# Kernel tuning notes

Hardware: AMD Instinct MI355X
Metric: run time of the kernel (lower is better)

## Reference

```python
import jax, jax.numpy as jnp
import numpy as np

B, S, H, P, L, O, E = 32, 1024, 256, 96, 200, 200, 64
N_EULER = 4


def setup_inputs() -> dict:
    key = jax.random.key(0)
    ks = jax.random.split(key, 20)
    def w(k, shape, fan_in):
        return jax.random.normal(k, shape, dtype=jnp.float32) / np.float32(np.sqrt(fan_in))
    return {
        'eco_data': jax.random.normal(ks[0], (B, E), dtype=jnp.float32),
        'tran_data': jax.random.normal(ks[1], (B, S, H), dtype=jnp.float32),
        'tran_data_label': jax.random.normal(ks[2], (B, P, 1), dtype=jnp.float32),
        'time_x': jax.random.uniform(ks[3], (B, S, 1), dtype=jnp.float32),
        'time_y': jax.random.uniform(ks[4], (B, P, 1), dtype=jnp.float32),
        'alpha': jnp.ones((1,), dtype=jnp.float32),
        'W_eco': w(ks[5], (E, H), E), 'b_eco': jnp.zeros((H,), jnp.float32),
        'W_in': w(ks[6], (3, H, L), H), 'W_t': w(ks[7], (3, 1, L), 1), 'b_in': jnp.zeros((3, L), jnp.float32),
        'W_f1': w(ks[8], (3, L, O), L), 'b_f1': jnp.zeros((3, O), jnp.float32),
        'W_f2': w(ks[9], (3, O, L), O), 'b_f2': jnp.zeros((3, L), jnp.float32),
        'W_out': w(ks[10], (3, L, H), L), 'b_out': jnp.zeros((3, H), jnp.float32),
        'W_lin': w(ks[11], (H, P), H), 'b_lin': jnp.zeros((P,), jnp.float32),
    }


def reference(eco_data, tran_data, tran_data_label, time_x, time_y, alpha,
              W_eco, b_eco, W_in, W_t, b_in, W_f1, b_f1, W_f2, b_f2,
              W_out, b_out, W_lin, b_lin):
    S_ = tran_data.shape[1]
    # eco_model: linear encoder [B, E] -> [B, H]
    eco_vec = eco_data @ W_eco + b_eco
    # time features over the observed window (concat then slice, per original)
    time_f = jnp.concatenate([time_x, time_y], axis=1)[:, :S_, :]  # [B, S, 1]
    # ODE_RNN for Q/K/V, stacked on k=3: encode -> Euler ODE solve -> readout
    h = jnp.tanh(jnp.einsum('bsh,khl->kbsl', tran_data, W_in)
                 + jnp.einsum('bst,ktl->kbsl', time_f, W_t)
                 + b_in[:, None, None, :])  # [3, B, S, L]
    dt = jnp.float32(1.0 / N_EULER)
    for _ in range(N_EULER):  # fixed-step Euler solve of tanh-MLP vector field
        hid = jnp.tanh(jnp.einsum('kbsl,klo->kbso', h, W_f1) + b_f1[:, None, None, :])
        f = jnp.einsum('kbso,kol->kbsl', hid, W_f2) + b_f2[:, None, None, :]
        h = h + dt * f
    qkv = (jnp.einsum('kbsl,klh->kbsh', h, W_out) + b_out[:, None, None, :]
           + eco_vec[None, :, None, :])  # [3, B, S, H]
    # zero out padded timesteps (last channel == 0 means padding)
    mask = jnp.where(tran_data[:, :, -1] == 0, 0.0, 1.0)[None, :, :, None]
    qkv = qkv * mask
    Q, K, V = qkv[0], qkv[1], qkv[2]
    scale = jnp.float32(1.0 / np.sqrt(H))
    scores = jnp.einsum('bqh,bkh->bqk', Q, K) * scale  # [B, S, S]
    attn = jax.nn.softmax(scores, axis=-1)
    ctx = jnp.einsum('bqk,bkh->bqh', attn, V)  # [B, S, H]
    out = ctx @ W_lin + b_lin  # [B, S, P]
    return out
```

## Files before the change

kernel.cpp:

```cpp
#include <hip/hip_runtime.h>

constexpr int Bc = 32, Sc = 1024, Hc = 256, Pc = 96, Lc = 200, Oc = 200, Ec = 64;
constexpr int Mtot = Bc * Sc;
constexpr float DT = 0.25f;
constexpr int KP = 224;

enum { MODE_ENC = 0, MODE_QKV = 3, MODE_OUT = 4, MODE_BF16OUT = 5 };

typedef short bf16x8 __attribute__((ext_vector_type(8)));
typedef float f32x4 __attribute__((ext_vector_type(4)));
typedef unsigned short u16x8 __attribute__((ext_vector_type(8)));
typedef unsigned int u32x2 __attribute__((ext_vector_type(2)));

__device__ inline unsigned short f2bf(float x) {
    union { float f; unsigned int u; } v; v.f = x;
    unsigned int r = v.u + 0x7FFFu + ((v.u >> 16) & 1u);
    return (unsigned short)(r >> 16);
}
__device__ inline float bf2f(unsigned short x) {
    union { unsigned int u; float f; } v; v.u = ((unsigned int)x) << 16;
    return v.f;
}
__device__ inline float fast_tanh(float x) {
    float e = __expf(2.f * x);
    float r = __frcp_rn(e + 1.f);
    return fmaf(-2.f, r, 1.f);
}
__device__ inline unsigned int cvt_pk_bf16(float a, float b) {
    unsigned int r;
    asm("v_cvt_pk_bf16_f32 %0, %1, %2" : "=v"(r) : "v"(a), "v"(b));
    return r;
}

__global__ __launch_bounds__(256) void eco_kernel(
    const float* __restrict__ eco_data, const float* __restrict__ W_eco,
    const float* __restrict__ b_eco, float* __restrict__ eco_vec)
{
    const int b = blockIdx.x, h = threadIdx.x;
    float acc = b_eco[h];
    #pragma unroll
    for (int e = 0; e < Ec; e++)
        acc = fmaf(eco_data[b * Ec + e], W_eco[(size_t)e * Hc + h], acc);
    eco_vec[(size_t)b * Hc + h] = acc;
}

__global__ void wtrans_all(
    const float* __restrict__ W_in, const float* __restrict__ W_f1,
    const float* __restrict__ W_f2, const float* __restrict__ W_out,
    const float* __restrict__ W_lin,
    unsigned short* __restrict__ WinT, unsigned short* __restrict__ Wf1T,
    unsigned short* __restrict__ Wf2T, unsigned short* __restrict__ WoutT,
    unsigned short* __restrict__ WlinT)
{
    const int z = blockIdx.z;
    const int n = blockIdx.x * 16 + threadIdx.x;
    const int k = blockIdx.y * 16 + threadIdx.y;

    const float* W; unsigned short* WT;
    int K, N, Kpad, Npad;
    if (z < 3)       { W = W_in  + (size_t)z * 256 * 200;       WT = WinT  + (size_t)z * 256 * 256;       K = 256; N = 200; Kpad = 256; Npad = 256; }
    else if (z < 6)  { W = W_f1  + (size_t)(z - 3) * 200 * 200; WT = Wf1T  + (size_t)(z - 3) * 224 * 256; K = 200; N = 200; Kpad = 224; Npad = 256; }
    else if (z < 9)  { W = W_f2  + (size_t)(z - 6) * 200 * 200; WT = Wf2T  + (size_t)(z - 6) * 224 * 256; K = 200; N = 200; Kpad = 224; Npad = 256; }
    else if (z < 12) { W = W_out + (size_t)(z - 9) * 200 * 256; WT = WoutT + (size_t)(z - 9) * 224 * 256; K = 200; N = 256; Kpad = 224; Npad = 256; }
    else             { W = W_lin;                               WT = WlinT;                               K = 256; N =  96; Kpad = 256; Npad = 128; }

    if (n >= Npad || k >= Kpad) return;
    float v = (n < N && k < K) ? W[(size_t)k * N + n] : 0.f;
    WT[(size_t)n * Kpad + k] = f2bf(v);
}

template <int MODE, typename TA>
__global__ __launch_bounds__(256) void mfma_gemm(
    const TA* __restrict__ A, const unsigned short* __restrict__ WT,
    const float* __restrict__ bias, void* __restrict__ Cv,
    int M, int N, int K, int Kpad,
    size_t aStrideZ, size_t wStrideZ, size_t bStrideZ, size_t cStrideZ,
    const float* __restrict__ timev, const float* __restrict__ wtv,
    const float* __restrict__ eco, const float* __restrict__ trandat,
    unsigned short* __restrict__ Ck, unsigned short* __restrict__ Cvt)
{
    constexpr int LDS_S = 40;
    constexpr int HALF = 128 * LDS_S;
    __shared__ unsigned short SM[4 * HALF];

    const int tid = threadIdx.x;
    const int z = blockIdx.z;
    const int m0 = blockIdx.y * 128;
    const int n0 = blockIdx.x * 128;

    A    += (size_t)z * aStrideZ;
    WT   += (size_t)z * wStrideZ;
    bias += (size_t)z * bStrideZ;
    float* Cf = (float*)Cv + (size_t)z * cStrideZ;
    unsigned short* Cu = (unsigned short*)Cv + (size_t)z * cStrideZ;
    const float* wtp = wtv ? (wtv + (size_t)z * Lc) : nullptr;

    const int lane = tid & 63, wave = tid >> 6;
    const int wm = (wave & 1) * 64, wn = (wave >> 1) * 64;
    const int fm = lane & 15, fq = lane >> 4;

    f32x4 acc[4][4];
    #pragma unroll
    for (int i = 0; i < 4; i++)
        #pragma unroll
        for (int j = 0; j < 4; j++)
            acc[i][j] = (f32x4){0.f, 0.f, 0.f, 0.f};

    float4  paf[4];
    ushort4 pau[4];
    u16x8   pb[2];

    auto LOAD = [&](int k0) {
        #pragma unroll
        for (int i = 0; i < 4; i++) {
            const int f = i * 256 + tid;
            const int row = f >> 3, kq = f & 7;
            if constexpr (sizeof(TA) == 4)
                paf[i] = *(const float4*)((const float*)A + (size_t)(m0 + row) * K + k0 + kq * 4);
            else
                pau[i] = *(const ushort4*)((const unsigned short*)A + (size_t)(m0 + row) * K + k0 + kq * 4);
        }
        #pragma unroll
        for (int i = 0; i < 2; i++) {
            const int f = i * 256 + tid;
            const int row = f >> 2, q = f & 3;
            pb[i] = *(const u16x8*)(WT + (size_t)(n0 + row) * Kpad + k0 + q * 8);
        }
    };
    auto STORE = [&](int buf) {
        unsigned short* Asd = SM + buf * 2 * HALF;
        unsigned short* Bsd = Asd + HALF;
        #pragma unroll
        for (int i = 0; i < 4; i++) {
            const int f = i * 256 + tid;
            const int row = f >> 3, kq = f & 7;
            ushort4 s;
            if constexpr (sizeof(TA) == 4) {
                s.x = f2bf(paf[i].x); s.y = f2bf(paf[i].y);
                s.z = f2bf(paf[i].z); s.w = f2bf(paf[i].w);
            } else {
                s = pau[i];
            }
            *(ushort4*)&Asd[row * LDS_S + kq * 4] = s;
        }
        #pragma unroll
        for (int i = 0; i < 2; i++) {
            const int f = i * 256 + tid;
            const int row = f >> 2, q = f & 3;
            *(u16x8*)&Bsd[row * LDS_S + q * 8] = pb[i];
        }
    };

    const int nk = K >> 5;
    LOAD(0);
    STORE(0);

    for (int ki = 0; ki < nk; ki++) {
        __syncthreads();
        const unsigned short* Asr = SM + (ki & 1) * 2 * HALF;
        const unsigned short* Bsr = Asr + HALF;

        if (ki + 1 < nk) LOAD((ki + 1) * 32);

        bf16x8 af[4], bfr[4];
        #pragma unroll
        for (int mi = 0; mi < 4; mi++)
            af[mi] = *(const bf16x8*)&Asr[(wm + mi * 16 + fm) * LDS_S + fq * 8];
        #pragma unroll
        for (int nj = 0; nj < 4; nj++)
            bfr[nj] = *(const bf16x8*)&Bsr[(wn + nj * 16 + fm) * LDS_S + fq * 8];
        #pragma unroll
        for (int mi = 0; mi < 4; mi++)
            #pragma unroll
            for (int nj = 0; nj < 4; nj++)
                acc[mi][nj] = __builtin_amdgcn_mfma_f32_16x16x32_bf16(
                    af[mi], bfr[nj], acc[mi][nj], 0, 0, 0);

        if (ki + 1 < nk) STORE((ki + 1) & 1);
    }

    if (MODE == MODE_QKV && z == 2) {
        constexpr int BSTR = 136;
        const int bq = m0 >> 10, sq0 = m0 & (Sc - 1);
        const int myhalf = wn >> 6;
        #pragma unroll
        for (int half = 0; half < 2; half++) {
            __syncthreads();
            if (myhalf == half) {
                #pragma unroll
                for (int mi = 0; mi < 4; mi++)
                    #pragma unroll
                    for (int nj = 0; nj < 4; nj++) {
                        const int nn = n0 + wn + nj * 16 + fm;
                        const float bv = bias[nn];
                        const float ev = eco[(size_t)bq * Hc + nn];
                        #pragma unroll
                        for (int r = 0; r < 4; r++) {
                            const int mm = m0 + wm + mi * 16 + fq * 4 + r;
                            float v = acc[mi][nj][r] + bv + ev;
                            if (trandat[(size_t)mm * Hc + (Hc - 1)] == 0.f) v = 0.f;
                            SM[(nj * 16 + fm) * BSTR + wm + mi * 16 + fq * 4 + r] = f2bf(v);
                        }
                    }
            }
            __syncthreads();
            #pragma unroll
            for (int i = 0; i < 4; i++) {
                const int vv = i * 256 + tid;
                const int nl = vv >> 4, vc = vv & 15;
                *(u16x8*)&Cvt[((size_t)bq * Hc + n0 + half * 64 + nl) * Sc + sq0 + vc * 8] =
                    *(const u16x8*)&SM[nl * BSTR + vc * 8];
            }
        }
        return;
    }

    #pragma unroll
    for (int mi = 0; mi < 4; mi++) {
        #pragma unroll
        for (int nj = 0; nj < 4; nj++) {
            const int nn = n0 + wn + nj * 16 + fm;
            if (nn >= N) continue;
            const float bv = (MODE == MODE_BF16OUT) ? 0.f
                           : ((MODE == MODE_ENC && nn >= Lc) ? 0.f : bias[nn]);
            #pragma unroll
            for (int r = 0; r < 4; r++) {
                const int mm = m0 + wm + mi * 16 + fq * 4 + r;
                float v = acc[mi][nj][r] + bv;
                if (MODE == MODE_ENC) {
                    float vv = (nn < Lc) ? fast_tanh(v + timev[mm] * wtp[nn]) : 0.f;
                    Cu[(size_t)mm * N + nn] = f2bf(vv);
                } else if (MODE == MODE_QKV) {
                    v += eco[(size_t)(mm >> 10) * Hc + nn];
                    if (trandat[(size_t)mm * Hc + (Hc - 1)] == 0.f) v = 0.f;
                    if (z == 0)      ((unsigned short*)Cv)[(size_t)mm * Hc + nn] = f2bf(v * 0.0625f);
                    else             Ck[(size_t)mm * Hc + nn] = f2bf(v);
                } else if (MODE == MODE_BF16OUT) {
                    Cu[(size_t)mm * N + nn] = f2bf(v);
                } else {
                    Cf[(size_t)mm * N + nn] = v;
                }
            }
        }
    }
}

__global__ __launch_bounds__(512, 2) void euler_fused(
    unsigned short* __restrict__ hg,
    const unsigned short* __restrict__ W1,
    const unsigned short* __restrict__ W2,
    const float* __restrict__ b1g, const float* __restrict__ b2g)
{
    constexpr int HS = 232;
    constexpr int WS = 40;
    extern __shared__ unsigned short lds[];
    unsigned short* hs  = lds;
    unsigned short* wsb[2] = { lds + 29696, lds + 38656 };
    unsigned short* hcb[2] = { lds + 47616, lds + 52736 };
    float* bs = (float*)(lds + 57856);

    const int tid = threadIdx.x;
    const int z = blockIdx.y;
    const int m0 = blockIdx.x * 128;
    unsigned short* hrow = hg + ((size_t)z * Mtot + m0) * KP;
    const unsigned short* W1z = W1 + (size_t)z * 256 * KP;
    const unsigned short* W2z = W2 + (size_t)z * 256 * KP;

    const int lane = tid & 63, w = tid >> 6;
    const int wm = (w & 3) * 32, wn = (w >> 2) * 112;
    const int fm = lane & 15, fq = lane >> 4;

    const int sr = tid >> 2, sq = tid & 3;
    const bool s2 = (tid < 384);

    if (tid < 448) {
        float v;
        if (tid < 224) v = (tid < Oc) ? b1g[z * Oc + tid] : 0.f;
        else { const int t = tid - 224; v = (t < Lc) ? b2g[z * Lc + t] : 0.f; }
        bs[tid] = v;
    }

    u16x8 pr0, pr1;
    pr0 = *(const u16x8*)&W1z[sr * KP + sq * 8];
    if (s2) pr1 = *(const u16x8*)&W1z[(sr + 128) * KP + sq * 8];

    #pragma unroll
    for (int i = 0; i < 7; i++) {
        const int f = i * 512 + tid;
        const int r = f / 28, c = (f % 28) * 8;
        *(u16x8*)&hs[r * HS + c] = *(const u16x8*)&hrow[(size_t)r * KP + c];
    }

    for (int it = 0; it < 4; it++) {
        __syncthreads();
        *(u16x8*)&wsb[0][sr * WS + sq * 8] = pr0;
        if (s2) *(u16x8*)&wsb[0][(sr + 128) * WS + sq * 8] = pr1;
        pr0 = *(const u16x8*)&W1z[sr * KP + 32 + sq * 8];
        if (s2) pr1 = *(const u16x8*)&W1z[(sr + 128) * KP + 32 + sq * 8];
        __syncthreads();

        f32x4 acc[2][7];
        #pragma unroll
        for (int mi = 0; mi < 2; mi++)
            #pragma unroll
            for (int nj = 0; nj < 7; nj++)
                acc[mi][nj] = (f32x4){0.f, 0.f, 0.f, 0.f};

        for (int k = 0; k < 7; k++) {
            if (k < 6) {
                unsigned short* wb = wsb[(k + 1) & 1];
                *(u16x8*)&wb[sr * WS + sq * 8] = pr0;
                if (s2) *(u16x8*)&wb[(sr + 128) * WS + sq * 8] = pr1;
                const unsigned short* src = (k + 2 < 7) ? (W1z + (k + 2) * 32) : W2z;
                pr0 = *(const u16x8*)&src[sr * KP + sq * 8];
                if (s2) pr1 = *(const u16x8*)&src[(sr + 128) * KP + sq * 8];
            }
            const unsigned short* wr = wsb[k & 1];
            bf16x8 af[2], bfr[7];
            #pragma unroll
            for (int mi = 0; mi < 2; mi++)
                af[mi] = *(const bf16x8*)&hs[(wm + mi * 16 + fm) * HS + k * 32 + fq * 8];
            #pragma unroll
            for (int nj = 0; nj < 7; nj++)
                bfr[nj] = *(const bf16x8*)&wr[(wn + nj * 16 + fm) * WS + fq * 8];
            #pragma unroll
            for (int mi = 0; mi < 2; mi++)
                #pragma unroll
                for (int nj = 0; nj < 7; nj++)
                    acc[mi][nj] = __builtin_amdgcn_mfma_f32_16x16x32_bf16(
                        bfr[nj], af[mi], acc[mi][nj], 0, 0, 0);
            __syncthreads();
        }

        unsigned int hidp[2][7][2];
        #pragma unroll
        for (int nj = 0; nj < 7; nj++) {
            const f32x4 b1v = *(const f32x4*)&bs[wn + nj * 16 + fq * 4];
            #pragma unroll
            for (int mi = 0; mi < 2; mi++) {
                const float t0 = fast_tanh(acc[mi][nj][0] + b1v[0]);
                const float t1 = fast_tanh(acc[mi][nj][1] + b1v[1]);
                const float t2 = fast_tanh(acc[mi][nj][2] + b1v[2]);
                const float t3 = fast_tanh(acc[mi][nj][3] + b1v[3]);
                hidp[mi][nj][0] = cvt_pk_bf16(t0, t1);
                hidp[mi][nj][1] = cvt_pk_bf16(t2, t3);
            }
        }

        {
            *(u16x8*)&wsb[0][sr * WS + sq * 8] = pr0;
            if (s2) *(u16x8*)&wsb[0][(sr + 128) * WS + sq * 8] = pr1;
            pr0 = *(const u16x8*)&W2z[sr * KP + 32 + sq * 8];
            if (s2) pr1 = *(const u16x8*)&W2z[(sr + 128) * KP + 32 + sq * 8];
            #pragma unroll
            for (int t2 = 0; t2 < 2; t2++) {
                const int c0 = t2 * 16;
                if (c0 >= wn && c0 < wn + 112) {
                    const int nj = (c0 - wn) >> 4;
                    #pragma unroll
                    for (int mi = 0; mi < 2; mi++) {
                        u32x2 p; p[0] = hidp[mi][nj][0]; p[1] = hidp[mi][nj][1];
                        *(u32x2*)&hcb[0][(wm + mi * 16 + fm) * WS + t2 * 16 + fq * 4] = p;
                    }
                }
            }
        }
        __syncthreads();

        f32x4 fac[2][7];
        #pragma unroll
        for (int mi = 0; mi < 2; mi++)
            #pragma unroll
            for (int nj = 0; nj < 7; nj++)
                fac[mi][nj] = (f32x4){0.f, 0.f, 0.f, 0.f};

        for (int k = 0; k < 7; k++) {
            if (k < 6) {
                unsigned short* wb = wsb[(k + 1) & 1];
                unsigned short* hb = hcb[(k + 1) & 1];
                *(u16x8*)&wb[sr * WS + sq * 8] = pr0;
                if (s2) *(u16x8*)&wb[(sr + 128) * WS + sq * 8] = pr1;
                if (k + 2 < 7) {
                    pr0 = *(const u16x8*)&W2z[sr * KP + (k + 2) * 32 + sq * 8];
                    if (s2) pr1 = *(const u16x8*)&W2z[(sr + 128) * KP + (k + 2) * 32 + sq * 8];
                } else if (it != 3) {
                    pr0 = *(const u16x8*)&W1z[sr * KP + sq * 8];
                    if (s2) pr1 = *(const u16x8*)&W1z[(sr + 128) * KP + sq * 8];
                }
                #pragma unroll
                for (int t2 = 0; t2 < 2; t2++) {
                    const int c0 = (k + 1) * 32 + t2 * 16;
                    if (c0 >= wn && c0 < wn + 112) {
                        const int nj = (c0 - wn) >> 4;
                        #pragma unroll
                        for (int mi = 0; mi < 2; mi++) {
                            u32x2 p; p[0] = hidp[mi][nj][0]; p[1] = hidp[mi][nj][1];
                            *(u32x2*)&hb[(wm + mi * 16 + fm) * WS + t2 * 16 + fq * 4] = p;
                        }
                    }
                }
            }
            const unsigned short* wr = wsb[k & 1];
            const unsigned short* hr = hcb[k & 1];
            bf16x8 af2[2], bf2[7];
            #pragma unroll
            for (int mi = 0; mi < 2; mi++)
                af2[mi] = *(const bf16x8*)&hr[(wm + mi * 16 + fm) * WS + fq * 8];
            #pragma unroll
            for (int nj = 0; nj < 7; nj++)
                bf2[nj] = *(const bf16x8*)&wr[(wn + nj * 16 + fm) * WS + fq * 8];
            #pragma unroll
            for (int mi = 0; mi < 2; mi++)
                #pragma unroll
                for (int nj = 0; nj < 7; nj++)
                    fac[mi][nj] = __builtin_amdgcn_mfma_f32_16x16x32_bf16(
                        bf2[nj], af2[mi], fac[mi][nj], 0, 0, 0);
            __syncthreads();
        }

        #pragma unroll
        for (int nj = 0; nj < 7; nj++) {
            const int n = wn + nj * 16 + fq * 4;
            const f32x4 b2v = *(const f32x4*)&bs[224 + n];
            #pragma unroll
            for (int mi = 0; mi < 2; mi++) {
                const int m = wm + mi * 16 + fm;
                const ushort4 hv = *(const ushort4*)&hs[m * HS + n];
                const float v0 = bf2f(hv.x) + DT * (fac[mi][nj][0] + b2v[0]);
                const float v1 = bf2f(hv.y) + DT * (fac[mi][nj][1] + b2v[1]);
                const float v2 = bf2f(hv.z) + DT * (fac[mi][nj][2] + b2v[2]);
                const float v3 = bf2f(hv.w) + DT * (fac[mi][nj][3] + b2v[3]);
                u32x2 p; p[0] = cvt_pk_bf16(v0, v1); p[1] = cvt_pk_bf16(v2, v3);
                *(u32x2*)&hs[m * HS + n] = p;
            }
        }
    }

    __syncthreads();
    #pragma unroll
    for (int i = 0; i < 7; i++) {
        const int f = i * 512 + tid;
        const int r = f / 28, c = (f % 28) * 8;
        *(u16x8*)&hrow[(size_t)r * KP + c] = *(const u16x8*)&hs[r * HS + c];
    }
}

__global__ __launch_bounds__(512) void flash_attn(
    const unsigned short* __restrict__ Qb, const unsigned short* __restrict__ Kb,
    const unsigned short* __restrict__ VT, unsigned short* __restrict__ ctx)
{
    constexpr int QS = 264;
    constexpr int KS = 264;
    constexpr int VS = 72;
    constexpr int PS = 72;
    extern __shared__ unsigned short lds[];
    unsigned short* qs = lds;
    unsigned short* ks = lds + 128 * QS;
    unsigned short* vs = lds + 128 * QS + 64 * KS;
    unsigned short* ps = lds + 128 * QS + 64 * KS + 256 * VS;

    const int tid = threadIdx.x;
    const int b = blockIdx.y, q0 = blockIdx.x * 128;
    const int lane = tid & 63, w = tid >> 6;
    const int fm = lane & 15, fq = lane >> 4;
    unsigned short* psw = ps + w * 16 * PS;

    const unsigned short* Qp = Qb + (size_t)b * Sc * Hc;
    const unsigned short* Kp = Kb + (size_t)b * Sc * Hc;
    const unsigned short* Vp = VT + (size_t)b * Hc * Sc;

    #pragma unroll
    for (int i = 0; i < 8; i++) {
        const int v = i * 512 + tid;
        *(u16x8*)&qs[(v >> 5) * QS + (v & 31) * 8] =
            *(const u16x8*)&Qp[(size_t)(q0 + (v >> 5)) * Hc + (v & 31) * 8];
    }

    f32x4 of[16];
    #pragma unroll
    for (int nj = 0; nj < 16; nj++) of[nj] = (f32x4){0.f, 0.f, 0.f, 0.f};
    float lrun[4] = {0.f, 0.f, 0.f, 0.f};

    for (int c = 0; c < 16; c++) {
        __syncthreads();
        const int s0 = c * 64;
        #pragma unroll
        for (int i = 0; i < 4; i++) {
            const int v = i * 512 + tid;
            *(u16x8*)&ks[(v >> 5) * KS + (v & 31) * 8] =
                *(const u16x8*)&Kp[(size_t)(s0 + (v >> 5)) * Hc + (v & 31) * 8];
            *(u16x8*)&vs[(v >> 3) * VS + (v & 7) * 8] =
                *(const u16x8*)&Vp[(size_t)(v >> 3) * Sc + s0 + (v & 7) * 8];
        }
        __syncthreads();

        f32x4 sc[4];
        #pragma unroll
        for (int nj = 0; nj < 4; nj++) sc[nj] = (f32x4){0.f, 0.f, 0.f, 0.f};
        #pragma unroll
        for (int kc = 0; kc < 8; kc++) {
            const bf16x8 aq = *(const bf16x8*)&qs[(w * 16 + fm) * QS + kc * 32 + fq * 8];
            #pragma unroll
            for (int nj = 0; nj < 4; nj++) {
                const bf16x8 bk = *(const bf16x8*)&ks[(nj * 16 + fm) * KS + kc * 32 + fq * 8];
                sc[nj] = __builtin_amdgcn_mfma_f32_16x16x32_bf16(aq, bk, sc[nj], 0, 0, 0);
            }
        }

        float rsum[4] = {0.f, 0.f, 0.f, 0.f};
        #pragma unroll
        for (int nj = 0; nj < 4; nj++)
            #pragma unroll
            for (int r = 0; r < 4; r++) {
                const float p = __expf(sc[nj][r]);
                rsum[r] += p;
                psw[(fq * 4 + r) * PS + nj * 16 + fm] = f2bf(p);
            }
        #pragma unroll
        for (int r = 0; r < 4; r++) {
            float s = rsum[r];
            #pragma unroll
            for (int o = 8; o > 0; o >>= 1) s += __shfl_xor(s, o, 64);
            lrun[r] += s;
        }

        #pragma unroll
        for (int t = 0; t < 2; t++) {
            const bf16x8 ap = *(const bf16x8*)&psw[fm * PS + t * 32 + fq * 8];
            #pragma unroll
            for (int nj = 0; nj < 16; nj++) {
                const bf16x8 bv = *(const bf16x8*)&vs[(nj * 16 + fm) * VS + t * 32 + fq * 8];
                of[nj] = __builtin_amdgcn_mfma_f32_16x16x32_bf16(ap, bv, of[nj], 0, 0, 0);
            }
        }
    }

    float inv[4];
    #pragma unroll
    for (int r = 0; r < 4; r++) inv[r] = __frcp_rn(lrun[r]);
    #pragma unroll
    for (int nj = 0; nj < 16; nj++)
        #pragma unroll
        for (int r = 0; r < 4; r++)
            ctx[((size_t)b * Sc + q0 + w * 16 + fq * 4 + r) * Hc + nj * 16 + fm] =
                f2bf(of[nj][r] * inv[r]);
}

extern "C" void kernel_launch(void* const* d_in, const int* in_sizes, int n_in,
                              void* d_out, int out_size, void* d_ws, size_t ws_size,
                              hipStream_t stream)
{
    const float* eco_data = (const float*)d_in[0];
    const float* tran     = (const float*)d_in[1];
    const float* time_x   = (const float*)d_in[3];
    const float* W_eco    = (const float*)d_in[6];
    const float* b_eco    = (const float*)d_in[7];
    const float* W_in     = (const float*)d_in[8];
    const float* W_t      = (const float*)d_in[9];
    const float* b_in     = (const float*)d_in[10];
    const float* W_f1     = (const float*)d_in[11];
    const float* b_f1     = (const float*)d_in[12];
    const float* W_f2     = (const float*)d_in[13];
    const float* b_f2     = (const float*)d_in[14];
    const float* W_out    = (const float*)d_in[15];
    const float* b_out    = (const float*)d_in[16];
    const float* W_lin    = (const float*)d_in[17];
    const float* b_lin    = (const float*)d_in[18];
    float* out = (float*)d_out;

    float* eco_vec = (float*)d_ws;
    unsigned short* hpad = (unsigned short*)(eco_vec + 8192);
    unsigned short* Qb = hpad + (size_t)3 * Mtot * KP;
    unsigned short* Kb = Qb + (size_t)Mtot * Hc;
    unsigned short* VT = Kb + (size_t)Mtot * Hc;
    unsigned short* P  = VT + (size_t)Mtot * Hc;
    unsigned short* WinT  = P + (size_t)Mtot * Sc;
    unsigned short* Wf1T  = WinT  + (size_t)3 * 256 * 256;
    unsigned short* Wf2T  = Wf1T  + (size_t)3 * 256 * KP;
    unsigned short* WoutT = Wf2T  + (size_t)3 * 256 * KP;
    unsigned short* WlinT = WoutT + (size_t)3 * 256 * KP;
    unsigned short* ctxb = hpad;

    constexpr int EULER_LDS = 57856 * 2 + 448 * 4;
    static_assert(EULER_LDS == 117504, "euler lds");
    hipFuncSetAttribute((const void*)euler_fused,
                        hipFuncAttributeMaxDynamicSharedMemorySize, EULER_LDS);
    constexpr int FLASH_LDS = (128 * 264 + 64 * 264 + 256 * 72 + 8 * 16 * 72) * 2;
    static_assert(FLASH_LDS == 156672, "flash lds");
    hipFuncSetAttribute((const void*)flash_attn,
                        hipFuncAttributeMaxDynamicSharedMemorySize, FLASH_LDS);

    eco_kernel<<<Bc, Hc, 0, stream>>>(eco_data, W_eco, b_eco, eco_vec);

    wtrans_all<<<dim3(16, 16, 13), dim3(16, 16), 0, stream>>>(
        W_in, W_f1, W_f2, W_out, W_lin, WinT, Wf1T, Wf2T, WoutT, WlinT);

    const dim3 blk(256);

    mfma_gemm<MODE_ENC, float><<<dim3(2, 256, 3), blk, 0, stream>>>(
        tran, WinT, b_in, hpad, Mtot, KP, Hc, 256,
        0, 65536, Lc, (size_t)Mtot * KP, time_x, W_t, nullptr, nullptr, nullptr, nullptr);

    euler_fused<<<dim3(Mtot / 128, 3), 512, EULER_LDS, stream>>>(
        hpad, Wf1T, Wf2T, b_f1, b_f2);

    mfma_gemm<MODE_QKV, unsigned short><<<dim3(2, 256, 3), blk, 0, stream>>>(
        hpad, WoutT, b_out, Qb, Mtot, Hc, KP, KP,
        (size_t)Mtot * KP, 57344, Hc, 0, nullptr, nullptr, eco_vec, tran, Kb, VT);

    flash_attn<<<dim3(8, 32), 512, FLASH_LDS, stream>>>(Qb, Kb, VT, ctxb);

    mfma_gemm<MODE_OUT, unsigned short><<<dim3(1, 256, 1), blk, 0, stream>>>(
        ctxb, WlinT, b_lin, out, Mtot, Pc, Hc, 256,
        0, 0, 0, 0, nullptr, nullptr, nullptr, nullptr, nullptr, nullptr);
}
```

Before: 458.8 us.

## Double-buffer K/V tiles via registers and keep Q fragments in registers in flash attention

```diff
diff --git a/kernel.cpp b/kernel.cpp
--- a/kernel.cpp
+++ b/kernel.cpp
@@ -449,15 +449,12 @@
     const unsigned short* __restrict__ Qb, const unsigned short* __restrict__ Kb,
     const unsigned short* __restrict__ VT, unsigned short* __restrict__ ctx)
 {
-    constexpr int QS = 264;
     constexpr int KS = 264;
     constexpr int VS = 72;
     constexpr int PS = 72;
+    constexpr int BUF = 64 * KS + 256 * VS;
     extern __shared__ unsigned short lds[];
-    unsigned short* qs = lds;
-    unsigned short* ks = lds + 128 * QS;
-    unsigned short* vs = lds + 128 * QS + 64 * KS;
-    unsigned short* ps = lds + 128 * QS + 64 * KS + 256 * VS;
+    unsigned short* ps = lds + 2 * BUF;
 
     const int tid = threadIdx.x;
     const int b = blockIdx.y, q0 = blockIdx.x * 128;
@@ -469,41 +466,56 @@
     const unsigned short* Kp = Kb + (size_t)b * Sc * Hc;
     const unsigned short* Vp = VT + (size_t)b * Hc * Sc;
 
-    #pragma unroll
-    for (int i = 0; i < 8; i++) {
-        const int v = i * 512 + tid;
-        *(u16x8*)&qs[(v >> 5) * QS + (v & 31) * 8] =
-            *(const u16x8*)&Qp[(size_t)(q0 + (v >> 5)) * Hc + (v & 31) * 8];
-    }
+    bf16x8 aq[8];
+    #pragma unroll
+    for (int kc = 0; kc < 8; kc++)
+        aq[kc] = *(const bf16x8*)&Qp[(size_t)(q0 + w * 16 + fm) * Hc + kc * 32 + fq * 8];
+
+    u16x8 kreg[4], vreg[4];
+    auto LOADC = [&](int c) {
+        const int s0 = c * 64;
+        #pragma unroll
+        for (int i = 0; i < 4; i++) {
+            const int v = i * 512 + tid;
+            kreg[i] = *(const u16x8*)&Kp[(size_t)(s0 + (v >> 5)) * Hc + (v & 31) * 8];
+            vreg[i] = *(const u16x8*)&Vp[(size_t)(v >> 3) * Sc + s0 + (v & 7) * 8];
+        }
+    };
+    auto STOREC = [&](int buf) {
+        unsigned short* ksd = lds + buf * BUF;
+        unsigned short* vsd = ksd + 64 * KS;
+        #pragma unroll
+        for (int i = 0; i < 4; i++) {
+            const int v = i * 512 + tid;
+            *(u16x8*)&ksd[(v >> 5) * KS + (v & 31) * 8] = kreg[i];
+            *(u16x8*)&vsd[(v >> 3) * VS + (v & 7) * 8] = vreg[i];
+        }
+    };
 
     f32x4 of[16];
     #pragma unroll
     for (int nj = 0; nj < 16; nj++) of[nj] = (f32x4){0.f, 0.f, 0.f, 0.f};
     float lrun[4] = {0.f, 0.f, 0.f, 0.f};
 
+    LOADC(0);
+    STOREC(0);
+
     for (int c = 0; c < 16; c++) {
         __syncthreads();
-        const int s0 = c * 64;
-        #pragma unroll
-        for (int i = 0; i < 4; i++) {
-            const int v = i * 512 + tid;
-            *(u16x8*)&ks[(v >> 5) * KS + (v & 31) * 8] =
-                *(const u16x8*)&Kp[(size_t)(s0 + (v >> 5)) * Hc + (v & 31) * 8];
-            *(u16x8*)&vs[(v >> 3) * VS + (v & 7) * 8] =
-                *(const u16x8*)&Vp[(size_t)(v >> 3) * Sc + s0 + (v & 7) * 8];
-        }
-        __syncthreads();
+        const unsigned short* ksr = lds + (c & 1) * BUF;
+        const unsigned short* vsr = ksr + 64 * KS;
+
+        if (c + 1 < 16) LOADC(c + 1);
 
         f32x4 sc[4];
         #pragma unroll
         for (int nj = 0; nj < 4; nj++) sc[nj] = (f32x4){0.f, 0.f, 0.f, 0.f};
         #pragma unroll
         for (int kc = 0; kc < 8; kc++) {
-            const bf16x8 aq = *(const bf16x8*)&qs[(w * 16 + fm) * QS + kc * 32 + fq * 8];
             #pragma unroll
             for (int nj = 0; nj < 4; nj++) {
-                const bf16x8 bk = *(const bf16x8*)&ks[(nj * 16 + fm) * KS + kc * 32 + fq * 8];
-                sc[nj] = __builtin_amdgcn_mfma_f32_16x16x32_bf16(aq, bk, sc[nj], 0, 0, 0);
+                const bf16x8 bk = *(const bf16x8*)&ksr[(nj * 16 + fm) * KS + kc * 32 + fq * 8];
+                sc[nj] = __builtin_amdgcn_mfma_f32_16x16x32_bf16(aq[kc], bk, sc[nj], 0, 0, 0);
             }
         }
 
@@ -529,10 +541,12 @@
             const bf16x8 ap = *(const bf16x8*)&psw[fm * PS + t * 32 + fq * 8];
             #pragma unroll
             for (int nj = 0; nj < 16; nj++) {
-                const bf16x8 bv = *(const bf16x8*)&vs[(nj * 16 + fm) * VS + t * 32 + fq * 8];
+                const bf16x8 bv = *(const bf16x8*)&vsr[(nj * 16 + fm) * VS + t * 32 + fq * 8];
                 of[nj] = __builtin_amdgcn_mfma_f32_16x16x32_bf16(ap, bv, of[nj], 0, 0, 0);
             }
         }
+
+        if (c + 1 < 16) STOREC((c + 1) & 1);
     }
 
     float inv[4];
@@ -585,8 +599,8 @@
     static_assert(EULER_LDS == 117504, "euler lds");
     hipFuncSetAttribute((const void*)euler_fused,
                         hipFuncAttributeMaxDynamicSharedMemorySize, EULER_LDS);
-    constexpr int FLASH_LDS = (128 * 264 + 64 * 264 + 256 * 72 + 8 * 16 * 72) * 2;
-    static_assert(FLASH_LDS == 156672, "flash lds");
+    constexpr int FLASH_LDS = (2 * (64 * 264 + 256 * 72) + 8 * 16 * 72) * 2;
+    static_assert(FLASH_LDS == 159744, "flash lds");
     hipFuncSetAttribute((const void*)flash_attn,
                         hipFuncAttributeMaxDynamicSharedMemorySize, FLASH_LDS);
 
```

Result: slower. 497.2 us (median of 2 runs) (+8.4%).
